# Kernel optimization log

Measured on AMD Instinct MI355X. Metric: run time of the kernel, lower is better.

Reference implementation:

```python
import jax, jax.numpy as jnp
import numpy as np

UP = 2      # up_ratio
K = 3       # kernel_size
EPS = 1e-5  # BatchNorm eps


def _bn(x, g, b, m, v):
    # eval-mode BatchNorm2d over channel axis 1 of NCHW
    scale = g / jnp.sqrt(v + EPS)
    return x * scale[:, None, None] + (b - m * scale)[:, None, None]


def setup_inputs() -> dict:
    key = jax.random.key(0)
    ks = jax.random.split(key, 13)
    N, C, H, W = 8, 256, 64, 64
    OC = 64
    P = UP * UP * K * K  # 36 encoder output channels
    return {
        "x": jax.random.normal(ks[0], (N, C, H, W), jnp.float32),
        "w0": jax.random.normal(ks[1], (OC, C), jnp.float32) * 0.05,
        "b0": jax.random.normal(ks[2], (OC,), jnp.float32) * 0.05,
        "bn0_g": jax.random.uniform(ks[3], (OC,), jnp.float32, 0.5, 1.5),
        "bn0_b": jax.random.normal(ks[4], (OC,), jnp.float32) * 0.05,
        "bn0_m": jax.random.normal(ks[5], (OC,), jnp.float32) * 0.05,
        "bn0_v": jax.random.uniform(ks[6], (OC,), jnp.float32, 0.5, 1.5),
        "w1": jax.random.normal(ks[7], (P, OC), jnp.float32) * 0.05,
        "b1": jax.random.normal(ks[8], (P,), jnp.float32) * 0.05,
        "bn1_g": jax.random.uniform(ks[9], (P,), jnp.float32, 0.5, 1.5),
        "bn1_b": jax.random.normal(ks[10], (P,), jnp.float32) * 0.05,
        "bn1_m": jax.random.normal(ks[11], (P,), jnp.float32) * 0.05,
        "bn1_v": jax.random.uniform(ks[12], (P,), jnp.float32, 0.5, 1.5),
    }


def reference(x, w0, b0, bn0_g, bn0_b, bn0_m, bn0_v,
              w1, b1, bn1_g, bn1_b, bn1_m, bn1_v):
    N, C, H, W = x.shape
    k2, u2 = K * K, UP * UP

    # layer0: 1x1 conv + BN + ReLU
    y = jnp.einsum('nchw,oc->nohw', x, w0) + b0[:, None, None]
    y = jax.nn.relu(_bn(y, bn0_g, bn0_b, bn0_m, bn0_v))

    # encoder: 1x1 conv + BN + ReLU -> (N, u2*k2, H, W)
    enc = jnp.einsum('nohw,po->nphw', y, w1) + b1[:, None, None]
    enc = jax.nn.relu(_bn(enc, bn1_g, bn1_b, bn1_m, bn1_v))

    # pixelshuffle(UP) + softmax over k2 + unfold back to low-res is
    # algebraically: split channels as (k2, u2) and softmax over k2.
    # channel index = k*u2 + r*UP + s, matching torch PixelShuffle layout.
    wts = jax.nn.softmax(enc.reshape(N, k2, u2, H, W), axis=1)  # n k u h w

    # im2col on input: ZeroPad2d(1) + 3x3 unfold -> (N, C, k2, H, W)
    pad = K // 2
    xp = jnp.pad(x, ((0, 0), (0, 0), (pad, pad), (pad, pad)))
    patches = jnp.stack([xp[:, :, i:i + H, j:j + W]
                         for i in range(K) for j in range(K)], axis=2)

    out = jnp.einsum('nckhw,nkuhw->ncuhw', patches, wts)  # (N, C, u2, H, W)

    # pixelshuffle: u = r*UP + s places value at (h*UP+r, w*UP+s)
    out = out.reshape(N, C, UP, UP, H, W)
    out = out.transpose(0, 1, 4, 2, 5, 3).reshape(N, C, H * UP, W * UP)
    return out
```

## Files before the change

### kernel.cpp

```cpp
#include <hip/hip_runtime.h>


#define EPS_BN 1e-5f

__global__ __launch_bounds__(256) void carafe_encoder(
    const float* __restrict__ x,
    const float* __restrict__ w0, const float* __restrict__ b0,
    const float* __restrict__ g0, const float* __restrict__ be0,
    const float* __restrict__ m0, const float* __restrict__ v0,
    const float* __restrict__ w1, const float* __restrict__ b1,
    const float* __restrict__ g1, const float* __restrict__ be1,
    const float* __restrict__ m1, const float* __restrict__ v1,
    float* __restrict__ wts)
{
    __shared__ float xs[128 * 64];
    __shared__ float wl[128 * 68];

    const int tid = threadIdx.x;
    const int b   = blockIdx.x;
    const int n   = b >> 6;
    const int hh  = b & 63;
    const int w   = tid & 63;
    const int og  = tid >> 6;

    float acc[16];
#pragma unroll
    for (int j = 0; j < 16; ++j) acc[j] = 0.f;

    for (int chunk = 0; chunk < 2; ++chunk) {
        const int c0 = chunk * 128;
        for (int idx = tid; idx < 128 * 64; idx += 256) {
            const int cc = idx >> 6, ww = idx & 63;
            xs[idx] = x[((n * 256 + c0 + cc) * 64 + hh) * 64 + ww];
        }
        for (int idx = tid; idx < 64 * 128; idx += 256) {
            const int o = idx >> 7, cc = idx & 127;
            wl[cc * 68 + o] = w0[o * 256 + c0 + cc];
        }
        __syncthreads();
#pragma unroll 4
        for (int cc = 0; cc < 128; ++cc) {
            const float xv = xs[cc * 64 + w];
            const float* wrow = &wl[cc * 68 + og * 16];
#pragma unroll
            for (int j = 0; j < 16; ++j)
                acc[j] = fmaf(xv, wrow[j], acc[j]);
        }
        __syncthreads();
    }

#pragma unroll
    for (int j = 0; j < 16; ++j) {
        const int o = og * 16 + j;
        const float sc = g0[o] * rsqrtf(v0[o] + EPS_BN);
        const float sh = (b0[o] - m0[o]) * sc + be0[o];
        xs[o * 64 + w] = fmaxf(fmaf(acc[j], sc, sh), 0.f);
    }
    for (int idx = tid; idx < 64 * 36; idx += 256) {
        const int o = idx / 36;
        const int p = idx - o * 36;
        wl[idx] = w1[p * 64 + o];
    }
    __syncthreads();

    float acc9[9];
#pragma unroll
    for (int kk = 0; kk < 9; ++kk) acc9[kk] = 0.f;
    const int u = og;
    for (int o = 0; o < 64; ++o) {
        const float yv = xs[o * 64 + w];
        const float* wrow = &wl[o * 36 + u];
#pragma unroll
        for (int kk = 0; kk < 9; ++kk)
            acc9[kk] = fmaf(yv, wrow[kk * 4], acc9[kk]);
    }

    float mx = -1e30f;
#pragma unroll
    for (int kk = 0; kk < 9; ++kk) {
        const int p = kk * 4 + u;
        const float sc = g1[p] * rsqrtf(v1[p] + EPS_BN);
        const float sh = (b1[p] - m1[p]) * sc + be1[p];
        float e = fmaxf(fmaf(acc9[kk], sc, sh), 0.f);
        acc9[kk] = e;
        mx = fmaxf(mx, e);
    }
    float s = 0.f;
#pragma unroll
    for (int kk = 0; kk < 9; ++kk) {
        acc9[kk] = __expf(acc9[kk] - mx);
        s += acc9[kk];
    }
    const float inv = 1.f / s;
#pragma unroll
    for (int kk = 0; kk < 9; ++kk)
        wts[((n * 36 + kk * 4 + u) * 64 + hh) * 64 + w] = acc9[kk] * inv;
}

__global__ __launch_bounds__(256) void carafe_reassemble(
    const float* __restrict__ x,
    const float* __restrict__ wts,
    float* __restrict__ out)
{
    const int t  = blockIdx.x * 256 + threadIdx.x;
    const int w  = t & 63;
    const int h  = (t >> 6) & 63;
    const int cg = (t >> 12) & 63;
    const int n  = t >> 18;

    float wt[36];
    const float* wp = wts + ((n * 36) * 64 + h) * 64 + w;
#pragma unroll
    for (int p = 0; p < 36; ++p) wt[p] = wp[p * 4096];

#pragma unroll
    for (int i = 0; i < 4; ++i) {
        const int c = cg * 4 + i;
        const float* xp = x + (n * 256 + c) * 4096;
        float a0 = 0.f, a1 = 0.f, a2 = 0.f, a3 = 0.f;
#pragma unroll
        for (int dh = -1; dh <= 1; ++dh) {
            const int hhp = h + dh;
            const bool hv = (hhp >= 0) & (hhp < 64);
#pragma unroll
            for (int dw = -1; dw <= 1; ++dw) {
                const int wwp = w + dw;
                const bool vv = hv & (wwp >= 0) & (wwp < 64);
                const float xv = vv ? xp[hhp * 64 + wwp] : 0.f;
                const int k = (dh + 1) * 3 + (dw + 1);
                a0 = fmaf(xv, wt[k * 4 + 0], a0);
                a1 = fmaf(xv, wt[k * 4 + 1], a1);
                a2 = fmaf(xv, wt[k * 4 + 2], a2);
                a3 = fmaf(xv, wt[k * 4 + 3], a3);
            }
        }
        float* op = out + ((n * 256 + c) * 128 + 2 * h) * 128 + 2 * w;
        float2 r0; r0.x = a0; r0.y = a1;
        float2 r1; r1.x = a2; r1.y = a3;
        *reinterpret_cast<float2*>(op)       = r0;
        *reinterpret_cast<float2*>(op + 128) = r1;
    }
}

extern "C" void kernel_launch(void* const* d_in, const int* in_sizes, int n_in,
                              void* d_out, int out_size, void* d_ws, size_t ws_size,
                              hipStream_t stream)
{
    const float* x   = (const float*)d_in[0];
    const float* w0  = (const float*)d_in[1];
    const float* b0  = (const float*)d_in[2];
    const float* g0  = (const float*)d_in[3];
    const float* be0 = (const float*)d_in[4];
    const float* m0  = (const float*)d_in[5];
    const float* v0  = (const float*)d_in[6];
    const float* w1  = (const float*)d_in[7];
    const float* b1  = (const float*)d_in[8];
    const float* g1  = (const float*)d_in[9];
    const float* be1 = (const float*)d_in[10];
    const float* m1  = (const float*)d_in[11];
    const float* v1  = (const float*)d_in[12];

    float* wts = (float*)d_ws;
    float* out = (float*)d_out;

    hipLaunchKernelGGL(carafe_encoder, dim3(512), dim3(256), 0, stream,
                       x, w0, b0, g0, be0, m0, v0, w1, b1, g1, be1, m1, v1, wts);
    hipLaunchKernelGGL(carafe_reassemble, dim3(8192), dim3(256), 0, stream,
                       x, wts, out);
}
```

Baseline: 214.3 us.

## Drop LDS staging in encoder, widen reassemble channel tile, use nontemporal stores

The encoder no longer stages x and w0 through shared memory. It reads x straight from global memory and reads the weights through wave-uniform (readfirstlane) addresses, so they can become scalar loads, and it removes the block barriers of the chunk loop. The w1 transpose into shared memory is gone for the same reason. The reassemble kernel now handles 8 channels per thread instead of 4, so the 36 softmax weights are reused over more channels at the cost of more registers and half as many blocks. Output stores are nontemporal to avoid cache pollution on the large write stream.

```diff
diff --git a/kernel.cpp b/kernel.cpp
--- a/kernel.cpp
+++ b/kernel.cpp
@@ -2,6 +2,8 @@
 
 
 #define EPS_BN 1e-5f
+
+typedef float f32x2 __attribute__((ext_vector_type(2)));
 
 __global__ __launch_bounds__(256) void carafe_encoder(
     const float* __restrict__ x,
@@ -13,40 +15,27 @@
     const float* __restrict__ m1, const float* __restrict__ v1,
     float* __restrict__ wts)
 {
-    __shared__ float xs[128 * 64];
-    __shared__ float wl[128 * 68];
+    __shared__ float ys[64 * 64];
 
     const int tid = threadIdx.x;
-    const int b   = blockIdx.x;
-    const int n   = b >> 6;
-    const int hh  = b & 63;
+    const int n   = blockIdx.x >> 6;
+    const int hh  = blockIdx.x & 63;
     const int w   = tid & 63;
-    const int og  = tid >> 6;
+    const int og  = __builtin_amdgcn_readfirstlane(tid >> 6);
 
     float acc[16];
 #pragma unroll
     for (int j = 0; j < 16; ++j) acc[j] = 0.f;
 
-    for (int chunk = 0; chunk < 2; ++chunk) {
-        const int c0 = chunk * 128;
-        for (int idx = tid; idx < 128 * 64; idx += 256) {
-            const int cc = idx >> 6, ww = idx & 63;
-            xs[idx] = x[((n * 256 + c0 + cc) * 64 + hh) * 64 + ww];
-        }
-        for (int idx = tid; idx < 64 * 128; idx += 256) {
-            const int o = idx >> 7, cc = idx & 127;
-            wl[cc * 68 + o] = w0[o * 256 + c0 + cc];
-        }
-        __syncthreads();
-#pragma unroll 4
-        for (int cc = 0; cc < 128; ++cc) {
-            const float xv = xs[cc * 64 + w];
-            const float* wrow = &wl[cc * 68 + og * 16];
+    const float* xp  = x + ((n * 256) * 64 + hh) * 64 + w;
+    const float* w0p = w0 + og * 16 * 256;
+
+#pragma unroll 8
+    for (int c = 0; c < 256; ++c) {
+        const float xv = xp[c * 4096];
 #pragma unroll
-            for (int j = 0; j < 16; ++j)
-                acc[j] = fmaf(xv, wrow[j], acc[j]);
-        }
-        __syncthreads();
+        for (int j = 0; j < 16; ++j)
+            acc[j] = fmaf(xv, w0p[j * 256 + c], acc[j]);
     }
 
 #pragma unroll
@@ -54,25 +43,21 @@
         const int o = og * 16 + j;
         const float sc = g0[o] * rsqrtf(v0[o] + EPS_BN);
         const float sh = (b0[o] - m0[o]) * sc + be0[o];
-        xs[o * 64 + w] = fmaxf(fmaf(acc[j], sc, sh), 0.f);
-    }
-    for (int idx = tid; idx < 64 * 36; idx += 256) {
-        const int o = idx / 36;
-        const int p = idx - o * 36;
-        wl[idx] = w1[p * 64 + o];
+        ys[o * 64 + w] = fmaxf(fmaf(acc[j], sc, sh), 0.f);
     }
     __syncthreads();
 
-    float acc9[9];
+    float e9[9];
 #pragma unroll
-    for (int kk = 0; kk < 9; ++kk) acc9[kk] = 0.f;
+    for (int kk = 0; kk < 9; ++kk) e9[kk] = 0.f;
     const int u = og;
+    const float* w1p = w1 + u * 64;
+#pragma unroll 4
     for (int o = 0; o < 64; ++o) {
-        const float yv = xs[o * 64 + w];
-        const float* wrow = &wl[o * 36 + u];
+        const float yv = ys[o * 64 + w];
 #pragma unroll
         for (int kk = 0; kk < 9; ++kk)
-            acc9[kk] = fmaf(yv, wrow[kk * 4], acc9[kk]);
+            e9[kk] = fmaf(yv, w1p[kk * 256 + o], e9[kk]);
     }
 
     float mx = -1e30f;
@@ -81,20 +66,20 @@
         const int p = kk * 4 + u;
         const float sc = g1[p] * rsqrtf(v1[p] + EPS_BN);
         const float sh = (b1[p] - m1[p]) * sc + be1[p];
-        float e = fmaxf(fmaf(acc9[kk], sc, sh), 0.f);
-        acc9[kk] = e;
+        float e = fmaxf(fmaf(e9[kk], sc, sh), 0.f);
+        e9[kk] = e;
         mx = fmaxf(mx, e);
     }
     float s = 0.f;
 #pragma unroll
     for (int kk = 0; kk < 9; ++kk) {
-        acc9[kk] = __expf(acc9[kk] - mx);
-        s += acc9[kk];
+        e9[kk] = __expf(e9[kk] - mx);
+        s += e9[kk];
     }
     const float inv = 1.f / s;
 #pragma unroll
     for (int kk = 0; kk < 9; ++kk)
-        wts[((n * 36 + kk * 4 + u) * 64 + hh) * 64 + w] = acc9[kk] * inv;
+        wts[((n * 36 + kk * 4 + u) * 64 + hh) * 64 + w] = e9[kk] * inv;
 }
 
 __global__ __launch_bounds__(256) void carafe_reassemble(
@@ -105,17 +90,17 @@
     const int t  = blockIdx.x * 256 + threadIdx.x;
     const int w  = t & 63;
     const int h  = (t >> 6) & 63;
-    const int cg = (t >> 12) & 63;
-    const int n  = t >> 18;
+    const int cg = (t >> 12) & 31;
+    const int n  = t >> 17;
 
     float wt[36];
-    const float* wp = wts + ((n * 36) * 64 + h) * 64 + w;
+    const float* wp = wts + (n * 36) * 4096 + h * 64 + w;
 #pragma unroll
     for (int p = 0; p < 36; ++p) wt[p] = wp[p * 4096];
 
 #pragma unroll
-    for (int i = 0; i < 4; ++i) {
-        const int c = cg * 4 + i;
+    for (int i = 0; i < 8; ++i) {
+        const int c = cg * 8 + i;
         const float* xp = x + (n * 256 + c) * 4096;
         float a0 = 0.f, a1 = 0.f, a2 = 0.f, a3 = 0.f;
 #pragma unroll
@@ -135,10 +120,10 @@
             }
         }
         float* op = out + ((n * 256 + c) * 128 + 2 * h) * 128 + 2 * w;
-        float2 r0; r0.x = a0; r0.y = a1;
-        float2 r1; r1.x = a2; r1.y = a3;
-        *reinterpret_cast<float2*>(op)       = r0;
-        *reinterpret_cast<float2*>(op + 128) = r1;
+        f32x2 r0; r0.x = a0; r0.y = a1;
+        f32x2 r1; r1.x = a2; r1.y = a3;
+        __builtin_nontemporal_store(r0, reinterpret_cast<f32x2*>(op));
+        __builtin_nontemporal_store(r1, reinterpret_cast<f32x2*>(op + 128));
     }
 }
 
@@ -165,6 +150,6 @@
 
     hipLaunchKernelGGL(carafe_encoder, dim3(512), dim3(256), 0, stream,
                        x, w0, b0, g0, be0, m0, v0, w1, b1, g1, be1, m1, v1, wts);
-    hipLaunchKernelGGL(carafe_reassemble, dim3(8192), dim3(256), 0, stream,
+    hipLaunchKernelGGL(carafe_reassemble, dim3(4096), dim3(256), 0, stream,
                        x, wts, out);
 }
```

After: 248.7 us. 1.16x slower.
